# Kernel tuning notes

Hardware: AMD Instinct MI355X
Metric: run time of the kernel (lower is better)

## Reference

```python
import jax, jax.numpy as jnp
import numpy as np

N_CLAUSES = 50000
FEAT_DIM = 64
EMBED_DIM = 128
NUM_QUEUES = 8
NUM_STEPS = 2048
ENTROPY_COEF = 0.1
ENTROPY_NORMALIZED = True
PASSIVE_PROB = 0.3  # expected passive-set fraction per selection step


def setup_inputs() -> dict:
    key = jax.random.key(0)
    ks = jax.random.split(key, 10)
    feature_vecs = jax.random.normal(ks[0], (N_CLAUSES, FEAT_DIM), dtype=jnp.float32)
    W1 = jax.random.normal(ks[1], (FEAT_DIM, EMBED_DIM), dtype=jnp.float32) / np.sqrt(FEAT_DIM)
    b1 = jnp.zeros((EMBED_DIM,), dtype=jnp.float32)
    W2 = jax.random.normal(ks[2], (EMBED_DIM, EMBED_DIM), dtype=jnp.float32) / np.sqrt(EMBED_DIM)
    b2 = jnp.zeros((EMBED_DIM,), dtype=jnp.float32)
    keys_w = jax.random.normal(ks[3], (NUM_QUEUES, EMBED_DIM), dtype=jnp.float32) / np.sqrt(EMBED_DIM)
    # Precomputed per-SEL-step reward: factor * (1/good_steps or 0 - TIME_PENALTY_MIXING * last_tim / tim_sum)
    rewards = jax.random.normal(ks[4], (NUM_STEPS,), dtype=jnp.float32) * 0.05
    # Passive-set membership mask per selection step (dynamic set flattened to masks)
    mask = jax.random.uniform(ks[5], (NUM_STEPS, N_CLAUSES)) < PASSIVE_PROB
    queue_idx = jnp.arange(NUM_STEPS, dtype=jnp.int32) % NUM_QUEUES  # time % NUM_EFFECTIVE_QUEUES
    sel_idx = jax.random.randint(ks[6], (NUM_STEPS,), 0, N_CLAUSES, dtype=jnp.int32)
    # the recorded (selected) clause must be in the passive set
    mask = mask.at[jnp.arange(NUM_STEPS), sel_idx].set(True)
    return {
        'feature_vecs': feature_vecs, 'W1': W1, 'b1': b1, 'W2': W2, 'b2': b2,
        'keys': keys_w, 'rewards': rewards, 'mask': mask,
        'queue_idx': queue_idx, 'sel_idx': sel_idx,
    }


def reference(feature_vecs, W1, b1, W2, b2, keys, rewards, mask, queue_idx, sel_idx):
    # clause_embedder: small MLP over clause features -> [N, E]
    h = jax.nn.relu(feature_vecs @ W1 + b1)
    emb = h @ W2 + b2
    # logits = clause_keys.weight @ embeddings.T -> [Q, N]
    logits = keys @ emb.T
    # per-step row of the selected queue: [S, N]
    rows = logits[queue_idx]
    neg_inf = jnp.asarray(-jnp.inf, dtype=rows.dtype)
    scores = jnp.where(mask, rows, neg_inf)
    lsm = jax.nn.log_softmax(scores, axis=1)  # masked entries stay -inf
    # cross_entropy = -lsm[cur_idx]
    ce = -lsm[jnp.arange(lsm.shape[0]), sel_idx]
    # minus_entropy = sum p * log p over passive members
    p_logp = jnp.where(mask, jnp.exp(lsm) * lsm, 0.0)
    minus_entropy = jnp.sum(p_logp, axis=1)
    if ENTROPY_NORMALIZED:
        count = jnp.sum(mask, axis=1).astype(lsm.dtype)
        minus_entropy = minus_entropy / jnp.log(count)
    loss = jnp.sum(rewards * ce) + ENTROPY_COEF * jnp.sum(minus_entropy)
    return loss.reshape(1)
```

## Files before the change

### kernel.cpp

```cpp
#include <hip/hip_runtime.h>
#include <hip/hip_bf16.h>

#define N_CLAUSES 50000
#define FEAT_DIM 64
#define EMBED_DIM 128
#define NUM_QUEUES 8
#define NUM_STEPS 2048
#define ENTROPY_COEF 0.1f

#define CHUNK 2048
#define NCHUNK 25
#define SGRP 4
#define KPG 64

typedef unsigned int v4u __attribute__((ext_vector_type(4)));
typedef unsigned int v2u __attribute__((ext_vector_type(2)));

#define WS_LOGITS 0
#define WS_ROWMAX 400000
#define WS_K2T    400008
#define WS_CQ     401032
#define WS_W1T    401040
#define WS_FLAG   409232
#define WS_PART   409248
#define WS_LOSS   (WS_PART + NCHUNK * NUM_STEPS * 4)

__device__ inline int enc_f(float f) {
  int b = __float_as_int(f);
  return b >= 0 ? b : (b ^ 0x7FFFFFFF);
}
__device__ inline float dec_f(int k) {
  return __int_as_float(k >= 0 ? k : (k ^ 0x7FFFFFFF));
}

__global__ __launch_bounds__(1024) void k_prep(const float* __restrict__ W1,
    const float* __restrict__ b2, const float* __restrict__ W2,
    const float* __restrict__ keys, const unsigned int* __restrict__ maskw,
    float* __restrict__ W1T, float* __restrict__ K2T, float* __restrict__ cq,
    int* __restrict__ flag, int* __restrict__ rowmax_i) {
  int tid = threadIdx.x;
  __shared__ int sflag;
  if (tid == 0) sflag = 0;
  __syncthreads();
  if (maskw[tid] > 1u) atomicOr(&sflag, 1);
  {
    int q = tid >> 7, j = tid & 127;
    float a = 0.f;
    for (int e = 0; e < EMBED_DIM; ++e)
      a = fmaf(W2[j * EMBED_DIM + e], keys[q * EMBED_DIM + e], a);
    K2T[j * 8 + q] = a;
  }
  if (tid < NUM_QUEUES) {
    float a = 0.f;
    for (int e = 0; e < EMBED_DIM; ++e)
      a = fmaf(b2[e], keys[tid * EMBED_DIM + e], a);
    cq[tid] = a;
    rowmax_i[tid] = (int)0x80000000;
  }
  for (int i = tid; i < FEAT_DIM * EMBED_DIM; i += 1024) {
    int j = i >> 6, f = i & 63;
    W1T[j * 64 + f] = W1[f * EMBED_DIM + j];
  }
  __syncthreads();
  if (tid == 0) *flag = sflag;
}

__global__ __launch_bounds__(64) void k_logits(const float* __restrict__ fv,
    const float* __restrict__ b1, const float* __restrict__ W1T,
    const float* __restrict__ K2T, const float* __restrict__ cq,
    float* __restrict__ logits, int* __restrict__ rowmax_i) {
  int t = threadIdx.x;
  int n = blockIdx.x * 64 + t;
  bool act = n < N_CLAUSES;
  int nn = act ? n : (N_CLAUSES - 1);
  float r[FEAT_DIM];
  const float4* fp = (const float4*)(fv + (size_t)nn * FEAT_DIM);
#pragma unroll
  for (int i = 0; i < FEAT_DIM / 4; ++i) {
    float4 v = fp[i];
    r[4 * i] = v.x; r[4 * i + 1] = v.y; r[4 * i + 2] = v.z; r[4 * i + 3] = v.w;
  }
  float acc[NUM_QUEUES];
#pragma unroll
  for (int q = 0; q < NUM_QUEUES; ++q) acc[q] = cq[q];
#pragma unroll 4
  for (int j = 0; j < EMBED_DIM; ++j) {
    const float* w = W1T + j * 64;
    float t0 = 0.f, t1 = 0.f, t2 = 0.f, t3 = 0.f;
#pragma unroll
    for (int f = 0; f < FEAT_DIM; f += 4) {
      t0 = fmaf(r[f],     w[f],     t0);
      t1 = fmaf(r[f + 1], w[f + 1], t1);
      t2 = fmaf(r[f + 2], w[f + 2], t2);
      t3 = fmaf(r[f + 3], w[f + 3], t3);
    }
    float tt = fmaxf((t0 + t1) + (t2 + t3) + b1[j], 0.f);
    const float* k2 = K2T + j * 8;
#pragma unroll
    for (int q = 0; q < NUM_QUEUES; ++q) acc[q] = fmaf(tt, k2[q], acc[q]);
  }
  if (act) {
#pragma unroll
    for (int q = 0; q < NUM_QUEUES; ++q) logits[(size_t)q * N_CLAUSES + n] = acc[q];
  }
  float mq = acc[0];
#pragma unroll
  for (int q = 1; q < NUM_QUEUES; ++q) {  }
  float red[NUM_QUEUES];
#pragma unroll
  for (int q = 0; q < NUM_QUEUES; ++q) {
    float m = acc[q];
#pragma unroll
    for (int o = 32; o > 0; o >>= 1) m = fmaxf(m, __shfl_xor(m, o, 64));
    red[q] = m;
  }
  if (t < NUM_QUEUES) atomicMax(&rowmax_i[t], enc_f(red[t]));
  (void)mq;
}

__global__ __launch_bounds__(256) void k_steps(const float* __restrict__ logits,
    const int* __restrict__ rowmax_i, const void* __restrict__ maskv,
    const int* __restrict__ flag, float4* __restrict__ part) {
  int chunk = blockIdx.x, q = blockIdx.y, g = blockIdx.z;
  int t = threadIdx.x, w = t >> 6;
  int base = chunk * CHUNK + 8 * t;
  bool act = base < N_CLAUSES;
  float M = dec_f(rowmax_i[q]);
  float e[8], es[8];
#pragma unroll
  for (int j = 0; j < 8; ++j) { e[j] = 0.f; es[j] = 0.f; }
  if (act) {
    const float* lrow = logits + (size_t)q * N_CLAUSES + base;
    float4 l0 = *(const float4*)(lrow);
    float4 l1 = *(const float4*)(lrow + 4);
    float a[8] = {l0.x - M, l0.y - M, l0.z - M, l0.w - M,
                  l1.x - M, l1.y - M, l1.z - M, l1.w - M};
#pragma unroll
    for (int j = 0; j < 8; ++j) { e[j] = __expf(a[j]); es[j] = e[j] * a[j]; }
  }
  int k0 = g * KPG + w;
  int s0 = q + 8 * k0;
  float4* pout = part + (size_t)chunk * NUM_STEPS;
  if (*flag != 0) {
    const unsigned char* mb = (const unsigned char*)maskv + (size_t)s0 * N_CLAUSES + base;
#pragma unroll 2
    for (int i = 0; i < 16; ++i) {
      float z = 0.f, s1 = 0.f, c = 0.f;
      if (act) {
        v2u m = __builtin_nontemporal_load((const v2u*)(mb + (size_t)32 * N_CLAUSES * i));
        unsigned mw[2] = {m.x, m.y};
#pragma unroll
        for (int h = 0; h < 2; ++h) {
#pragma unroll
          for (int k = 0; k < 4; ++k) {
            float bb = ((mw[h] >> (8 * k)) & 0xffu) ? 1.f : 0.f;
            int j = 4 * h + k;
            z = fmaf(bb, e[j], z);
            s1 = fmaf(bb, es[j], s1);
            c += bb;
          }
        }
      }
#pragma unroll
      for (int o = 32; o > 0; o >>= 1) {
        z += __shfl_xor(z, o, 64); s1 += __shfl_xor(s1, o, 64); c += __shfl_xor(c, o, 64);
      }
      if ((t & 63) == 0) pout[s0 + 32 * i] = make_float4(z, s1, c, 0.f);
    }
  } else {
    const int* mi = (const int*)maskv + (size_t)s0 * N_CLAUSES + base;
#pragma unroll 2
    for (int i = 0; i < 16; ++i) {
      float z = 0.f, s1 = 0.f, c = 0.f;
      if (act) {
        const int* p = mi + (size_t)32 * N_CLAUSES * i;
        v4u m0 = __builtin_nontemporal_load((const v4u*)p);
        v4u m1 = __builtin_nontemporal_load((const v4u*)(p + 4));
        unsigned mv[8] = {m0.x, m0.y, m0.z, m0.w, m1.x, m1.y, m1.z, m1.w};
#pragma unroll
        for (int j = 0; j < 8; ++j) {
          float bb = mv[j] ? 1.f : 0.f;
          z = fmaf(bb, e[j], z);
          s1 = fmaf(bb, es[j], s1);
          c += bb;
        }
      }
#pragma unroll
      for (int o = 32; o > 0; o >>= 1) {
        z += __shfl_xor(z, o, 64); s1 += __shfl_xor(s1, o, 64); c += __shfl_xor(c, o, 64);
      }
      if ((t & 63) == 0) pout[s0 + 32 * i] = make_float4(z, s1, c, 0.f);
    }
  }
}

__global__ __launch_bounds__(256) void k_red(const float4* __restrict__ part,
    const float* __restrict__ logits, const int* __restrict__ rowmax_i,
    const float* __restrict__ rewards, const int* __restrict__ qi,
    const int* __restrict__ si, float* __restrict__ loss) {
  int t = threadIdx.x, w = t >> 6, lane = t & 63;
  int s = blockIdx.x * 64 + lane;
  float z = 0.f, s1 = 0.f, c = 0.f;
  for (int e = w; e < NCHUNK; e += 4) {
    float4 p = part[(size_t)e * NUM_STEPS + s];
    z += p.x; s1 += p.y; c += p.z;
  }
  __shared__ float sZ[4][64], sS[4][64], sC[4][64];
  sZ[w][lane] = z; sS[w][lane] = s1; sC[w][lane] = c;
  __syncthreads();
  if (w == 0) {
    z  = sZ[0][lane] + sZ[1][lane] + sZ[2][lane] + sZ[3][lane];
    s1 = sS[0][lane] + sS[1][lane] + sS[2][lane] + sS[3][lane];
    c  = sC[0][lane] + sC[1][lane] + sC[2][lane] + sC[3][lane];
    int q = qi[s];
    float M = dec_f(rowmax_i[q]);
    float ssel = logits[(size_t)q * N_CLAUSES + si[s]];
    float logZ = logf(z);
    float ce = logZ - (ssel - M);
    float me = (s1 / z - logZ) / logf(c);
    loss[s] = rewards[s] * ce + ENTROPY_COEF * me;
  }
}

__global__ __launch_bounds__(256) void k_sum(const float* __restrict__ loss,
                                             float* __restrict__ out) {
  int tid = threadIdx.x;
  float v = 0.f;
  for (int i = tid; i < NUM_STEPS; i += 256) v += loss[i];
#pragma unroll
  for (int o = 32; o > 0; o >>= 1) v += __shfl_xor(v, o, 64);
  __shared__ float sv[4];
  if ((tid & 63) == 0) sv[tid >> 6] = v;
  __syncthreads();
  if (tid == 0) out[0] = sv[0] + sv[1] + sv[2] + sv[3];
}

extern "C" void kernel_launch(void* const* d_in, const int* in_sizes, int n_in,
                              void* d_out, int out_size, void* d_ws, size_t ws_size,
                              hipStream_t stream) {
  const float* fv      = (const float*)d_in[0];
  const float* W1      = (const float*)d_in[1];
  const float* b1      = (const float*)d_in[2];
  const float* W2      = (const float*)d_in[3];
  const float* b2      = (const float*)d_in[4];
  const float* keys    = (const float*)d_in[5];
  const float* rewards = (const float*)d_in[6];
  const void*  mask    = d_in[7];
  const int*   queue_i = (const int*)d_in[8];
  const int*   sel_i   = (const int*)d_in[9];
  float* out = (float*)d_out;
  float* ws  = (float*)d_ws;

  float*  logits   = ws + WS_LOGITS;
  int*    rowmax_i = (int*)(ws + WS_ROWMAX);
  float*  K2T      = ws + WS_K2T;
  float*  cq       = ws + WS_CQ;
  float*  W1T      = ws + WS_W1T;
  int*    flag     = (int*)(ws + WS_FLAG);
  float4* part     = (float4*)(ws + WS_PART);
  float*  loss     = ws + WS_LOSS;

  hipLaunchKernelGGL(k_prep, dim3(1), dim3(1024), 0, stream,
                     W1, b2, W2, keys, (const unsigned int*)mask, W1T, K2T, cq, flag, rowmax_i);
  hipLaunchKernelGGL(k_logits, dim3((N_CLAUSES + 63) / 64), dim3(64), 0, stream,
                     fv, b1, W1T, K2T, cq, logits, rowmax_i);
  hipLaunchKernelGGL(k_steps, dim3(NCHUNK, NUM_QUEUES, SGRP), dim3(256), 0, stream,
                     logits, rowmax_i, mask, flag, part);
  hipLaunchKernelGGL(k_red, dim3(NUM_STEPS / 64), dim3(256), 0, stream,
                     part, logits, rowmax_i, rewards, queue_i, sel_i, loss);
  hipLaunchKernelGGL(k_sum, dim3(1), dim3(256), 0, stream, loss, out);
}
```

Measured before the change: 148.9 us.

## Fuse all stages into one cooperative persistent kernel with grid syncs

Replaces five separate kernel launches with a single cooperative kernel of 400 blocks that uses grid-wide syncs between the prep, logits, per-step masked reduction and final loss phases. The logits phase now uses 256-thread blocks with a shared-memory max before the atomic. The step phase covers twice as many steps per block, so it runs with fewer, longer-running blocks. The final reduction runs in a single block. This removes launch gaps and inter-kernel overhead, but grid.sync costs time and the mask-streaming phase has less parallelism to hide memory latency.

```diff
diff --git a/kernel.cpp b/kernel.cpp
--- a/kernel.cpp
+++ b/kernel.cpp
@@ -1,5 +1,7 @@
 #include <hip/hip_runtime.h>
-#include <hip/hip_bf16.h>
+#include <hip/hip_cooperative_groups.h>
+
+namespace cg = cooperative_groups;
 
 #define N_CLAUSES 50000
 #define FEAT_DIM 64
@@ -8,10 +10,11 @@
 #define NUM_STEPS 2048
 #define ENTROPY_COEF 0.1f
 
+#define GRID_BLOCKS 400
+#define NB1 196
 #define CHUNK 2048
 #define NCHUNK 25
-#define SGRP 4
-#define KPG 64
+#define ILOOP 32
 
 typedef unsigned int v4u __attribute__((ext_vector_type(4)));
 typedef unsigned int v2u __attribute__((ext_vector_type(2)));
@@ -23,7 +26,14 @@
 #define WS_W1T    401040
 #define WS_FLAG   409232
 #define WS_PART   409248
-#define WS_LOSS   (WS_PART + NCHUNK * NUM_STEPS * 4)
+
+struct Params {
+  const float* fv; const float* W1; const float* b1; const float* W2;
+  const float* b2; const float* keys; const float* rewards;
+  const void* mask; const int* qi; const int* si;
+  float* W1T; float* K2T; float* cq; int* flag; int* rowmax_i;
+  float* logits; float4* part; float* out;
+};
 
 __device__ inline int enc_f(float f) {
   int b = __float_as_int(f);
@@ -33,240 +43,231 @@
   return __int_as_float(k >= 0 ? k : (k ^ 0x7FFFFFFF));
 }
 
-__global__ __launch_bounds__(1024) void k_prep(const float* __restrict__ W1,
-    const float* __restrict__ b2, const float* __restrict__ W2,
-    const float* __restrict__ keys, const unsigned int* __restrict__ maskw,
-    float* __restrict__ W1T, float* __restrict__ K2T, float* __restrict__ cq,
-    int* __restrict__ flag, int* __restrict__ rowmax_i) {
-  int tid = threadIdx.x;
-  __shared__ int sflag;
-  if (tid == 0) sflag = 0;
-  __syncthreads();
-  if (maskw[tid] > 1u) atomicOr(&sflag, 1);
+__global__ __launch_bounds__(256) void k_mega(Params p) {
+  cg::grid_group grid = cg::this_grid();
+  const int bid = blockIdx.x, t = threadIdx.x;
+  __shared__ float sred[4][8];
+  __shared__ float sv[4];
+
+  if (bid == 0) {
+    for (int i = t; i < FEAT_DIM * EMBED_DIM; i += 256) {
+      int j = i >> 6, f = i & 63;
+      p.W1T[j * 64 + f] = p.W1[f * EMBED_DIM + j];
+    }
+  } else if (bid == 1) {
+    for (int idx = t; idx < EMBED_DIM * NUM_QUEUES; idx += 256) {
+      int j = idx >> 3, q = idx & 7;
+      float a = 0.f;
+      for (int e = 0; e < EMBED_DIM; ++e)
+        a = fmaf(p.W2[j * EMBED_DIM + e], p.keys[q * EMBED_DIM + e], a);
+      p.K2T[idx] = a;
+    }
+  } else if (bid == 2) {
+    if (t < NUM_QUEUES) {
+      float a = 0.f;
+      for (int e = 0; e < EMBED_DIM; ++e)
+        a = fmaf(p.b2[e], p.keys[t * EMBED_DIM + e], a);
+      p.cq[t] = a;
+      p.rowmax_i[t] = (int)0x80000000;
+    }
+  } else if (bid == 3) {
+    __shared__ int sfl;
+    if (t == 0) sfl = 0;
+    __syncthreads();
+    const unsigned* mw = (const unsigned*)p.mask;
+    bool fl = (mw[t] > 1u) | (mw[t + 256] > 1u) | (mw[t + 512] > 1u) | (mw[t + 768] > 1u);
+    if (__any(fl) && (t & 63) == 0) atomicOr(&sfl, 1);
+    __syncthreads();
+    if (t == 0) *p.flag = sfl;
+  }
+
+  grid.sync();
+
+  if (bid < NB1) {
+    int n = bid * 256 + t;
+    bool act = n < N_CLAUSES;
+    int nn = act ? n : (N_CLAUSES - 1);
+    float r[FEAT_DIM];
+    const float4* fp = (const float4*)(p.fv + (size_t)nn * FEAT_DIM);
+#pragma unroll
+    for (int i = 0; i < FEAT_DIM / 4; ++i) {
+      float4 v = fp[i];
+      r[4 * i] = v.x; r[4 * i + 1] = v.y; r[4 * i + 2] = v.z; r[4 * i + 3] = v.w;
+    }
+    float acc[NUM_QUEUES];
+#pragma unroll
+    for (int q = 0; q < NUM_QUEUES; ++q) acc[q] = p.cq[q];
+#pragma unroll 4
+    for (int j = 0; j < EMBED_DIM; ++j) {
+      const float* w = p.W1T + j * 64;
+      float t0 = 0.f, t1 = 0.f, t2 = 0.f, t3 = 0.f;
+#pragma unroll
+      for (int f = 0; f < FEAT_DIM; f += 4) {
+        t0 = fmaf(r[f],     w[f],     t0);
+        t1 = fmaf(r[f + 1], w[f + 1], t1);
+        t2 = fmaf(r[f + 2], w[f + 2], t2);
+        t3 = fmaf(r[f + 3], w[f + 3], t3);
+      }
+      float tt = fmaxf((t0 + t1) + (t2 + t3) + p.b1[j], 0.f);
+      const float* k2 = p.K2T + j * 8;
+#pragma unroll
+      for (int q = 0; q < NUM_QUEUES; ++q) acc[q] = fmaf(tt, k2[q], acc[q]);
+    }
+    if (act) {
+#pragma unroll
+      for (int q = 0; q < NUM_QUEUES; ++q)
+        p.logits[(size_t)q * N_CLAUSES + n] = acc[q];
+    }
+    float red[NUM_QUEUES];
+#pragma unroll
+    for (int q = 0; q < NUM_QUEUES; ++q) {
+      float m = acc[q];
+#pragma unroll
+      for (int o = 32; o > 0; o >>= 1) m = fmaxf(m, __shfl_xor(m, o, 64));
+      red[q] = m;
+    }
+    if ((t & 63) == 0) {
+      int w = t >> 6;
+      sred[w][0] = red[0]; sred[w][1] = red[1]; sred[w][2] = red[2]; sred[w][3] = red[3];
+      sred[w][4] = red[4]; sred[w][5] = red[5]; sred[w][6] = red[6]; sred[w][7] = red[7];
+    }
+    __syncthreads();
+    if (t < NUM_QUEUES) {
+      float m = fmaxf(fmaxf(sred[0][t], sred[1][t]), fmaxf(sred[2][t], sred[3][t]));
+      atomicMax(&p.rowmax_i[t], enc_f(m));
+    }
+  }
+
+  grid.sync();
+
   {
-    int q = tid >> 7, j = tid & 127;
-    float a = 0.f;
-    for (int e = 0; e < EMBED_DIM; ++e)
-      a = fmaf(W2[j * EMBED_DIM + e], keys[q * EMBED_DIM + e], a);
-    K2T[j * 8 + q] = a;
-  }
-  if (tid < NUM_QUEUES) {
-    float a = 0.f;
-    for (int e = 0; e < EMBED_DIM; ++e)
-      a = fmaf(b2[e], keys[tid * EMBED_DIM + e], a);
-    cq[tid] = a;
-    rowmax_i[tid] = (int)0x80000000;
-  }
-  for (int i = tid; i < FEAT_DIM * EMBED_DIM; i += 1024) {
-    int j = i >> 6, f = i & 63;
-    W1T[j * 64 + f] = W1[f * EMBED_DIM + j];
-  }
-  __syncthreads();
-  if (tid == 0) *flag = sflag;
-}
-
-__global__ __launch_bounds__(64) void k_logits(const float* __restrict__ fv,
-    const float* __restrict__ b1, const float* __restrict__ W1T,
-    const float* __restrict__ K2T, const float* __restrict__ cq,
-    float* __restrict__ logits, int* __restrict__ rowmax_i) {
-  int t = threadIdx.x;
-  int n = blockIdx.x * 64 + t;
-  bool act = n < N_CLAUSES;
-  int nn = act ? n : (N_CLAUSES - 1);
-  float r[FEAT_DIM];
-  const float4* fp = (const float4*)(fv + (size_t)nn * FEAT_DIM);
-#pragma unroll
-  for (int i = 0; i < FEAT_DIM / 4; ++i) {
-    float4 v = fp[i];
-    r[4 * i] = v.x; r[4 * i + 1] = v.y; r[4 * i + 2] = v.z; r[4 * i + 3] = v.w;
-  }
-  float acc[NUM_QUEUES];
-#pragma unroll
-  for (int q = 0; q < NUM_QUEUES; ++q) acc[q] = cq[q];
-#pragma unroll 4
-  for (int j = 0; j < EMBED_DIM; ++j) {
-    const float* w = W1T + j * 64;
-    float t0 = 0.f, t1 = 0.f, t2 = 0.f, t3 = 0.f;
-#pragma unroll
-    for (int f = 0; f < FEAT_DIM; f += 4) {
-      t0 = fmaf(r[f],     w[f],     t0);
-      t1 = fmaf(r[f + 1], w[f + 1], t1);
-      t2 = fmaf(r[f + 2], w[f + 2], t2);
-      t3 = fmaf(r[f + 3], w[f + 3], t3);
-    }
-    float tt = fmaxf((t0 + t1) + (t2 + t3) + b1[j], 0.f);
-    const float* k2 = K2T + j * 8;
-#pragma unroll
-    for (int q = 0; q < NUM_QUEUES; ++q) acc[q] = fmaf(tt, k2[q], acc[q]);
-  }
-  if (act) {
-#pragma unroll
-    for (int q = 0; q < NUM_QUEUES; ++q) logits[(size_t)q * N_CLAUSES + n] = acc[q];
-  }
-  float mq = acc[0];
-#pragma unroll
-  for (int q = 1; q < NUM_QUEUES; ++q) {  }
-  float red[NUM_QUEUES];
-#pragma unroll
-  for (int q = 0; q < NUM_QUEUES; ++q) {
-    float m = acc[q];
-#pragma unroll
-    for (int o = 32; o > 0; o >>= 1) m = fmaxf(m, __shfl_xor(m, o, 64));
-    red[q] = m;
-  }
-  if (t < NUM_QUEUES) atomicMax(&rowmax_i[t], enc_f(red[t]));
-  (void)mq;
-}
-
-__global__ __launch_bounds__(256) void k_steps(const float* __restrict__ logits,
-    const int* __restrict__ rowmax_i, const void* __restrict__ maskv,
-    const int* __restrict__ flag, float4* __restrict__ part) {
-  int chunk = blockIdx.x, q = blockIdx.y, g = blockIdx.z;
-  int t = threadIdx.x, w = t >> 6;
-  int base = chunk * CHUNK + 8 * t;
-  bool act = base < N_CLAUSES;
-  float M = dec_f(rowmax_i[q]);
-  float e[8], es[8];
-#pragma unroll
-  for (int j = 0; j < 8; ++j) { e[j] = 0.f; es[j] = 0.f; }
-  if (act) {
-    const float* lrow = logits + (size_t)q * N_CLAUSES + base;
-    float4 l0 = *(const float4*)(lrow);
-    float4 l1 = *(const float4*)(lrow + 4);
-    float a[8] = {l0.x - M, l0.y - M, l0.z - M, l0.w - M,
-                  l1.x - M, l1.y - M, l1.z - M, l1.w - M};
-#pragma unroll
-    for (int j = 0; j < 8; ++j) { e[j] = __expf(a[j]); es[j] = e[j] * a[j]; }
-  }
-  int k0 = g * KPG + w;
-  int s0 = q + 8 * k0;
-  float4* pout = part + (size_t)chunk * NUM_STEPS;
-  if (*flag != 0) {
-    const unsigned char* mb = (const unsigned char*)maskv + (size_t)s0 * N_CLAUSES + base;
+    int chunk = bid % NCHUNK, rr = bid / NCHUNK;
+    int q = rr & 7, g = rr >> 3;
+    int w = t >> 6;
+    int base = chunk * CHUNK + 8 * t;
+    bool act = base < N_CLAUSES;
+    float M = dec_f(p.rowmax_i[q]);
+    float e[8], es[8];
+#pragma unroll
+    for (int j = 0; j < 8; ++j) { e[j] = 0.f; es[j] = 0.f; }
+    if (act) {
+      const float* lrow = p.logits + (size_t)q * N_CLAUSES + base;
+      float4 l0 = *(const float4*)(lrow);
+      float4 l1 = *(const float4*)(lrow + 4);
+      float a[8] = {l0.x - M, l0.y - M, l0.z - M, l0.w - M,
+                    l1.x - M, l1.y - M, l1.z - M, l1.w - M};
+#pragma unroll
+      for (int j = 0; j < 8; ++j) { e[j] = __expf(a[j]); es[j] = e[j] * a[j]; }
+    }
+    int k0 = g * 128 + w;
+    int s0 = q + 8 * k0;
+    float4* pout = p.part + (size_t)chunk * NUM_STEPS;
+    if (*p.flag != 0) {
+      const unsigned char* mb = (const unsigned char*)p.mask + (size_t)s0 * N_CLAUSES + base;
 #pragma unroll 2
-    for (int i = 0; i < 16; ++i) {
-      float z = 0.f, s1 = 0.f, c = 0.f;
-      if (act) {
-        v2u m = __builtin_nontemporal_load((const v2u*)(mb + (size_t)32 * N_CLAUSES * i));
-        unsigned mw[2] = {m.x, m.y};
-#pragma unroll
-        for (int h = 0; h < 2; ++h) {
-#pragma unroll
-          for (int k = 0; k < 4; ++k) {
-            float bb = ((mw[h] >> (8 * k)) & 0xffu) ? 1.f : 0.f;
-            int j = 4 * h + k;
+      for (int i = 0; i < ILOOP; ++i) {
+        float z = 0.f, s1 = 0.f, c = 0.f;
+        if (act) {
+          v2u m = __builtin_nontemporal_load((const v2u*)(mb + (size_t)32 * N_CLAUSES * i));
+          unsigned mw2[2] = {m.x, m.y};
+#pragma unroll
+          for (int h = 0; h < 2; ++h) {
+#pragma unroll
+            for (int k = 0; k < 4; ++k) {
+              float bb = ((mw2[h] >> (8 * k)) & 0xffu) ? 1.f : 0.f;
+              int j = 4 * h + k;
+              z = fmaf(bb, e[j], z);
+              s1 = fmaf(bb, es[j], s1);
+              c += bb;
+            }
+          }
+        }
+#pragma unroll
+        for (int o = 32; o > 0; o >>= 1) {
+          z += __shfl_xor(z, o, 64); s1 += __shfl_xor(s1, o, 64); c += __shfl_xor(c, o, 64);
+        }
+        if ((t & 63) == 0) pout[s0 + 32 * i] = make_float4(z, s1, c, 0.f);
+      }
+    } else {
+      const int* mi = (const int*)p.mask + (size_t)s0 * N_CLAUSES + base;
+#pragma unroll 2
+      for (int i = 0; i < ILOOP; ++i) {
+        float z = 0.f, s1 = 0.f, c = 0.f;
+        if (act) {
+          const int* pp = mi + (size_t)32 * N_CLAUSES * i;
+          v4u m0 = __builtin_nontemporal_load((const v4u*)pp);
+          v4u m1 = __builtin_nontemporal_load((const v4u*)(pp + 4));
+          unsigned mv[8] = {m0.x, m0.y, m0.z, m0.w, m1.x, m1.y, m1.z, m1.w};
+#pragma unroll
+          for (int j = 0; j < 8; ++j) {
+            float bb = mv[j] ? 1.f : 0.f;
             z = fmaf(bb, e[j], z);
             s1 = fmaf(bb, es[j], s1);
             c += bb;
           }
         }
-      }
-#pragma unroll
-      for (int o = 32; o > 0; o >>= 1) {
-        z += __shfl_xor(z, o, 64); s1 += __shfl_xor(s1, o, 64); c += __shfl_xor(c, o, 64);
-      }
-      if ((t & 63) == 0) pout[s0 + 32 * i] = make_float4(z, s1, c, 0.f);
-    }
-  } else {
-    const int* mi = (const int*)maskv + (size_t)s0 * N_CLAUSES + base;
+#pragma unroll
+        for (int o = 32; o > 0; o >>= 1) {
+          z += __shfl_xor(z, o, 64); s1 += __shfl_xor(s1, o, 64); c += __shfl_xor(c, o, 64);
+        }
+        if ((t & 63) == 0) pout[s0 + 32 * i] = make_float4(z, s1, c, 0.f);
+      }
+    }
+  }
+
+  grid.sync();
+
+  if (bid == 0) {
+    float lsum = 0.f;
 #pragma unroll 2
-    for (int i = 0; i < 16; ++i) {
+    for (int k = 0; k < 8; ++k) {
+      int s = (k << 8) | t;
       float z = 0.f, s1 = 0.f, c = 0.f;
-      if (act) {
-        const int* p = mi + (size_t)32 * N_CLAUSES * i;
-        v4u m0 = __builtin_nontemporal_load((const v4u*)p);
-        v4u m1 = __builtin_nontemporal_load((const v4u*)(p + 4));
-        unsigned mv[8] = {m0.x, m0.y, m0.z, m0.w, m1.x, m1.y, m1.z, m1.w};
-#pragma unroll
-        for (int j = 0; j < 8; ++j) {
-          float bb = mv[j] ? 1.f : 0.f;
-          z = fmaf(bb, e[j], z);
-          s1 = fmaf(bb, es[j], s1);
-          c += bb;
-        }
-      }
-#pragma unroll
-      for (int o = 32; o > 0; o >>= 1) {
-        z += __shfl_xor(z, o, 64); s1 += __shfl_xor(s1, o, 64); c += __shfl_xor(c, o, 64);
-      }
-      if ((t & 63) == 0) pout[s0 + 32 * i] = make_float4(z, s1, c, 0.f);
-    }
-  }
-}
-
-__global__ __launch_bounds__(256) void k_red(const float4* __restrict__ part,
-    const float* __restrict__ logits, const int* __restrict__ rowmax_i,
-    const float* __restrict__ rewards, const int* __restrict__ qi,
-    const int* __restrict__ si, float* __restrict__ loss) {
-  int t = threadIdx.x, w = t >> 6, lane = t & 63;
-  int s = blockIdx.x * 64 + lane;
-  float z = 0.f, s1 = 0.f, c = 0.f;
-  for (int e = w; e < NCHUNK; e += 4) {
-    float4 p = part[(size_t)e * NUM_STEPS + s];
-    z += p.x; s1 += p.y; c += p.z;
-  }
-  __shared__ float sZ[4][64], sS[4][64], sC[4][64];
-  sZ[w][lane] = z; sS[w][lane] = s1; sC[w][lane] = c;
-  __syncthreads();
-  if (w == 0) {
-    z  = sZ[0][lane] + sZ[1][lane] + sZ[2][lane] + sZ[3][lane];
-    s1 = sS[0][lane] + sS[1][lane] + sS[2][lane] + sS[3][lane];
-    c  = sC[0][lane] + sC[1][lane] + sC[2][lane] + sC[3][lane];
-    int q = qi[s];
-    float M = dec_f(rowmax_i[q]);
-    float ssel = logits[(size_t)q * N_CLAUSES + si[s]];
-    float logZ = logf(z);
-    float ce = logZ - (ssel - M);
-    float me = (s1 / z - logZ) / logf(c);
-    loss[s] = rewards[s] * ce + ENTROPY_COEF * me;
-  }
-}
-
-__global__ __launch_bounds__(256) void k_sum(const float* __restrict__ loss,
-                                             float* __restrict__ out) {
-  int tid = threadIdx.x;
-  float v = 0.f;
-  for (int i = tid; i < NUM_STEPS; i += 256) v += loss[i];
-#pragma unroll
-  for (int o = 32; o > 0; o >>= 1) v += __shfl_xor(v, o, 64);
-  __shared__ float sv[4];
-  if ((tid & 63) == 0) sv[tid >> 6] = v;
-  __syncthreads();
-  if (tid == 0) out[0] = sv[0] + sv[1] + sv[2] + sv[3];
+      for (int e2 = 0; e2 < NCHUNK; ++e2) {
+        float4 pp = p.part[(size_t)e2 * NUM_STEPS + s];
+        z += pp.x; s1 += pp.y; c += pp.z;
+      }
+      int q = p.qi[s];
+      float M = dec_f(p.rowmax_i[q]);
+      float ssel = p.logits[(size_t)q * N_CLAUSES + p.si[s]];
+      float logZ = logf(z);
+      float ce = logZ - (ssel - M);
+      float me = (s1 / z - logZ) / logf(c);
+      lsum += p.rewards[s] * ce + ENTROPY_COEF * me;
+    }
+#pragma unroll
+    for (int o = 32; o > 0; o >>= 1) lsum += __shfl_xor(lsum, o, 64);
+    if ((t & 63) == 0) sv[t >> 6] = lsum;
+    __syncthreads();
+    if (t == 0) p.out[0] = sv[0] + sv[1] + sv[2] + sv[3];
+  }
 }
 
 extern "C" void kernel_launch(void* const* d_in, const int* in_sizes, int n_in,
                               void* d_out, int out_size, void* d_ws, size_t ws_size,
                               hipStream_t stream) {
-  const float* fv      = (const float*)d_in[0];
-  const float* W1      = (const float*)d_in[1];
-  const float* b1      = (const float*)d_in[2];
-  const float* W2      = (const float*)d_in[3];
-  const float* b2      = (const float*)d_in[4];
-  const float* keys    = (const float*)d_in[5];
-  const float* rewards = (const float*)d_in[6];
-  const void*  mask    = d_in[7];
-  const int*   queue_i = (const int*)d_in[8];
-  const int*   sel_i   = (const int*)d_in[9];
-  float* out = (float*)d_out;
-  float* ws  = (float*)d_ws;
-
-  float*  logits   = ws + WS_LOGITS;
-  int*    rowmax_i = (int*)(ws + WS_ROWMAX);
-  float*  K2T      = ws + WS_K2T;
-  float*  cq       = ws + WS_CQ;
-  float*  W1T      = ws + WS_W1T;
-  int*    flag     = (int*)(ws + WS_FLAG);
-  float4* part     = (float4*)(ws + WS_PART);
-  float*  loss     = ws + WS_LOSS;
-
-  hipLaunchKernelGGL(k_prep, dim3(1), dim3(1024), 0, stream,
-                     W1, b2, W2, keys, (const unsigned int*)mask, W1T, K2T, cq, flag, rowmax_i);
-  hipLaunchKernelGGL(k_logits, dim3((N_CLAUSES + 63) / 64), dim3(64), 0, stream,
-                     fv, b1, W1T, K2T, cq, logits, rowmax_i);
-  hipLaunchKernelGGL(k_steps, dim3(NCHUNK, NUM_QUEUES, SGRP), dim3(256), 0, stream,
-                     logits, rowmax_i, mask, flag, part);
-  hipLaunchKernelGGL(k_red, dim3(NUM_STEPS / 64), dim3(256), 0, stream,
-                     part, logits, rowmax_i, rewards, queue_i, sel_i, loss);
-  hipLaunchKernelGGL(k_sum, dim3(1), dim3(256), 0, stream, loss, out);
-}
+  float* ws = (float*)d_ws;
+  Params prm;
+  prm.fv      = (const float*)d_in[0];
+  prm.W1      = (const float*)d_in[1];
+  prm.b1      = (const float*)d_in[2];
+  prm.W2      = (const float*)d_in[3];
+  prm.b2      = (const float*)d_in[4];
+  prm.keys    = (const float*)d_in[5];
+  prm.rewards = (const float*)d_in[6];
+  prm.mask    = d_in[7];
+  prm.qi      = (const int*)d_in[8];
+  prm.si      = (const int*)d_in[9];
+  prm.W1T     = ws + WS_W1T;
+  prm.K2T     = ws + WS_K2T;
+  prm.cq      = ws + WS_CQ;
+  prm.flag    = (int*)(ws + WS_FLAG);
+  prm.rowmax_i= (int*)(ws + WS_ROWMAX);
+  prm.logits  = ws + WS_LOGITS;
+  prm.part    = (float4*)(ws + WS_PART);
+  prm.out     = (float*)d_out;
+
+  void* args[] = {(void*)&prm};
+  hipLaunchCooperativeKernel((void*)k_mega, dim3(GRID_BLOCKS), dim3(256),
+                             args, 0, stream);
+}
```

Result: slower. 434.8 us (+192.1%).
